# Kernel optimization log

Hardware: AMD Instinct MI355X
Metric: run time of the kernel (lower is better)

Reference implementation:

```python
import jax, jax.numpy as jnp
import numpy as np

HEADS = 4


def setup_inputs() -> dict:
    key = jax.random.key(0)
    kx, kqkv, kbq, ko, kbo = jax.random.split(key, 5)
    B, C, H, W = 4, 256, 64, 64
    x = jax.random.normal(kx, (B, C, H, W), dtype=jnp.float32)
    # torch nn.Linear stores weight as [out_features, in_features]
    w_qkv = jax.random.normal(kqkv, (3 * C, C), dtype=jnp.float32) * (1.0 / np.sqrt(C))
    b_qkv = jax.random.normal(kbq, (3 * C,), dtype=jnp.float32) * 0.02
    w_o = jax.random.normal(ko, (C, C), dtype=jnp.float32) * (1.0 / np.sqrt(C))
    b_o = jax.random.normal(kbo, (C,), dtype=jnp.float32) * 0.02
    return {"x": x, "w_qkv": w_qkv, "b_qkv": b_qkv, "w_o": w_o, "b_o": b_o}


def reference(x, w_qkv, b_qkv, w_o, b_o):
    B, C, H, W = x.shape
    S = H * W
    hd = C // HEADS
    # (B, C, H, W) -> (B, S, C)
    xt = x.reshape(B, C, S).transpose(0, 2, 1)
    qkv = xt @ w_qkv.T + b_qkv                      # (B, S, 3C)
    q, k, v = jnp.split(qkv, 3, axis=-1)
    def to_heads(t):
        return t.reshape(B, S, HEADS, hd).transpose(0, 2, 1, 3)  # (B, h, S, hd)
    q, k, v = to_heads(q), to_heads(k), to_heads(v)
    scores = jnp.einsum('bhqd,bhkd->bhqk', q, k) / jnp.sqrt(jnp.float32(hd))
    attn = jax.nn.softmax(scores, axis=-1)          # dropout inactive (eval)
    out = jnp.einsum('bhqk,bhkd->bhqd', attn, v)    # (B, h, S, hd)
    out = out.transpose(0, 2, 1, 3).reshape(B, S, C)
    y = out @ w_o.T + b_o                            # (B, S, C)
    y = y.reshape(B, H, W, C).transpose(0, 3, 1, 2)  # (B, C, H, W)
    return y
```

## Files before the change

kernel.cpp:

```cpp
#include <hip/hip_runtime.h>
#include <stdint.h>

#define DI __device__ __forceinline__

typedef __attribute__((ext_vector_type(8))) __bf16 bf16x8;
typedef __attribute__((ext_vector_type(8))) unsigned short u16x8;
typedef __attribute__((ext_vector_type(4))) float f32x4;
typedef __attribute__((ext_vector_type(4))) uint32_t u32x4;
typedef unsigned short u16;

constexpr int Bb = 4, Cc = 256, Ss = 4096, HD = 64;
constexpr int ELEMS = Bb * Cc * Ss;

DI float bf2f(u16 h) { union { unsigned u; float f; } x; x.u = ((unsigned)h) << 16; return x.f; }
DI u16 f2bf(float f) {
  union { float f; unsigned u; } x; x.f = f;
  return (u16)((x.u + 0x7FFFu + ((x.u >> 16) & 1u)) >> 16);
}
DI uint32_t pack2bf_trunc(float a, float b) {
  union { float f; uint32_t u; } xa, xb;
  xa.f = a; xb.f = b;
  return __builtin_amdgcn_perm(xb.u, xa.u, 0x07060302u);
}
DI bf16x8 ldfrag(const u16* p) { return __builtin_bit_cast(bf16x8, *(const u16x8*)p); }

DI void g2l16(const u16* g, u16* l) {
  __builtin_amdgcn_global_load_lds((const __attribute__((address_space(1))) uint32_t*)(const void*)g,
                                   (__attribute__((address_space(3))) uint32_t*)(void*)l, 16, 0, 0);
}

__global__ __launch_bounds__(256) void k_transpose(const float* __restrict__ x, u16* __restrict__ xt,
                                                   const float* __restrict__ wq, const float* __restrict__ wo,
                                                   u16* __restrict__ wqb, u16* __restrict__ wob) {
  __shared__ u16 T[64][72];
  const int st = blockIdx.x, ct = blockIdx.y, b = blockIdx.z;
  const int tid = threadIdx.x;
  {
    int flat = blockIdx.x + 64 * blockIdx.y + 256 * blockIdx.z;
    int widx = flat * 256 + tid;
    if (widx < 196608) wqb[widx] = f2bf(wq[widx]);
    else wob[widx - 196608] = f2bf(wo[widx - 196608]);
  }
#pragma unroll
  for (int e = 0; e < 2; e++) {
    int ss = tid + e * 256;
    int r = ss >> 3, seg = ss & 7;
    size_t base = ((size_t)(b * Cc + ct * 64 + r) << 12) + st * 64 + seg * 8;
    const float4* xv = (const float4*)(x + base);
    float4 v0 = xv[0], v1 = xv[1];
    u16x8 t;
    t[0] = f2bf(v0.x); t[1] = f2bf(v0.y); t[2] = f2bf(v0.z); t[3] = f2bf(v0.w);
    t[4] = f2bf(v1.x); t[5] = f2bf(v1.y); t[6] = f2bf(v1.z); t[7] = f2bf(v1.w);
    *(u16x8*)&T[r][(seg ^ ((r >> 3) & 7)) * 8] = t;
  }
  __syncthreads();
#pragma unroll
  for (int e = 0; e < 2; e++) {
    int ss = tid + e * 256;
    int sr = ss >> 3, cseg = ss & 7;
    u16x8 o;
#pragma unroll
    for (int j = 0; j < 8; j++) {
      int row = cseg * 8 + j;
      o[j] = T[row][(((sr >> 3) ^ cseg) * 8) + (sr & 7)];
    }
    *(u16x8*)(xt + ((size_t)(b * Ss + st * 64 + sr) << 8) + ct * 64 + cseg * 8) = o;
  }
}

__global__ __launch_bounds__(256) void k_qkv(const u16* __restrict__ xt, const u16* __restrict__ w,
                                             const float* __restrict__ bias,
                                             u16* __restrict__ q, u16* __restrict__ kk_, u16* __restrict__ vt) {
  __shared__ union {
    u16 ab[2][2][128][32];
    u16 tile[128][136];
  } sm;
  const int tid = threadIdx.x;
  const int wv = tid >> 6, lane = tid & 63;
  const int wm = wv >> 1, wn = wv & 1;
  const int lr = lane & 15, quad = lane >> 4;
  const int r0 = blockIdx.x * 128;
  const int j0 = blockIdx.y * 128;

  const int srow = lane >> 2;
  const int sg = ((lane & 3) ^ (srow & 3)) * 8;
  const u16* pA[2];
  const u16* pB[2];
#pragma unroll
  for (int e = 0; e < 2; e++) {
    pA[e] = xt + (size_t)(r0 + e * 64 + wv * 16 + srow) * 256 + sg;
    pB[e] = w + (size_t)(j0 + e * 64 + wv * 16 + srow) * 256 + sg;
  }
  auto stage = [&](int buf, int k0) {
#pragma unroll
    for (int e = 0; e < 2; e++) {
      g2l16(pA[e] + k0, &sm.ab[buf][0][e * 64 + wv * 16][0]);
      g2l16(pB[e] + k0, &sm.ab[buf][1][e * 64 + wv * 16][0]);
    }
  };

  f32x4 acc[4][4] = {};
  stage(0, 0);
  __syncthreads();
  for (int ks = 0; ks < 8; ks++) {
    const int cur = ks & 1;
    if (ks < 7) stage(cur ^ 1, (ks + 1) * 32);
    bf16x8 a[4], b[4];
#pragma unroll
    for (int mt = 0; mt < 4; mt++)
      a[mt] = ldfrag(&sm.ab[cur][0][wm * 64 + mt * 16 + lr][(quad ^ (lr & 3)) * 8]);
#pragma unroll
    for (int nt = 0; nt < 4; nt++)
      b[nt] = ldfrag(&sm.ab[cur][1][wn * 64 + nt * 16 + lr][(quad ^ (lr & 3)) * 8]);
#pragma unroll
    for (int mt = 0; mt < 4; mt++)
#pragma unroll
      for (int nt = 0; nt < 4; nt++)
        acc[mt][nt] = __builtin_amdgcn_mfma_f32_16x16x32_bf16(a[mt], b[nt], acc[mt][nt], 0, 0, 0);
    __syncthreads();
  }

  float bj[4];
#pragma unroll
  for (int nt = 0; nt < 4; nt++) bj[nt] = bias[j0 + wn * 64 + nt * 16 + lr];
  __syncthreads();
  if (blockIdx.y < 4) {
    const int part = blockIdx.y >> 1;
    u16* outp = part ? kk_ : q;
    const float sc = part ? 1.0f : 0.18033688f;
#pragma unroll
    for (int nt = 0; nt < 4; nt++) {
      int lc = wn * 64 + nt * 16 + lr;
#pragma unroll
      for (int mt = 0; mt < 4; mt++)
#pragma unroll
        for (int rg = 0; rg < 4; rg++)
          sm.tile[wm * 64 + mt * 16 + quad * 4 + rg][lc] = f2bf((acc[mt][nt][rg] + bj[nt]) * sc);
    }
    __syncthreads();
    const int hb2 = (blockIdx.y & 1) * 2;
#pragma unroll
    for (int it = 0; it < 8; it++) {
      int seg = tid + it * 256;
      int row = seg >> 4, cs = seg & 15;
      u16x8 o = *(const u16x8*)&sm.tile[row][cs * 8];
      int head = hb2 + (cs >> 3), d0 = (cs & 7) * 8;
      int rr = r0 + row, b_ = rr >> 12, s = rr & 4095;
      *(u16x8*)(outp + ((size_t)((b_ * 4 + head) * Ss + s) << 6) + d0) = o;
    }
  } else {
    const int hb = (blockIdx.y - 4) * 2;
#pragma unroll
    for (int nt = 0; nt < 4; nt++) {
      int lc = wn * 64 + nt * 16 + lr;
#pragma unroll
      for (int mt = 0; mt < 4; mt++)
#pragma unroll
        for (int rg = 0; rg < 4; rg++)
          sm.tile[wm * 64 + mt * 16 + quad * 4 + rg][lc] = f2bf(acc[mt][nt][rg] + bj[nt]);
    }
    __syncthreads();
    const int b2 = r0 >> 12, sbase = r0 & 4095;
#pragma unroll
    for (int it = 0; it < 8; it++) {
      int seg = tid + it * 256;
      int sq = seg & 15, hd = seg >> 4;
      int c = sq >> 3, s8 = sq & 7;
      u16x8 o;
#pragma unroll
      for (int j = 0; j < 8; j++) {
        int slot = s8 * 8 + j;
        int sw = (((slot >> 5) & 1) << 5) | (((slot >> 2) & 1) << 4) |
                 (((slot >> 3) & 3) << 2) | (slot & 3);
        o[j] = sm.tile[c * 64 + sw][hd];
      }
      int head = hb + (hd >> 6), d = hd & 63;
      *(u16x8*)(vt + ((size_t)((b2 * 4 + head) * 64 + d) << 12) + sbase + c * 64 + s8 * 8) = o;
    }
  }
}

__global__ __launch_bounds__(512, 4) void k_attn(const u16* __restrict__ Q, const u16* __restrict__ K,
                                                 const u16* __restrict__ VT, u16* __restrict__ AO,
                                                 u16* __restrict__ AOP, float* __restrict__ lpart,
                                                 int nsplit) {
  __shared__ union {
    struct { u16 Kl[2][2][64][64]; u16 Vl[2][2][64][64]; } s;
    u16 W[8][32 * 72];
  } smem;
  const int tid = threadIdx.x;
  const int wv = tid >> 6, lane = tid & 63;
  const int lr = lane & 15, quad = lane >> 4;
  const int bh = blockIdx.y;
  const int b_ = bh >> 2, head = bh & 3;
  const int qbase = blockIdx.x * 256 + wv * 32;
  const int sp = blockIdx.z;
  const int nbig = 32 / nsplit, bg0 = sp * nbig;
  const u16* Qh = Q + (size_t)bh * Ss * HD;
  const u16* Kh = K + (size_t)bh * Ss * HD;
  const u16* Vh = VT + (size_t)bh * HD * Ss;

  bf16x8 qb[2][2];
#pragma unroll
  for (int nt = 0; nt < 2; nt++)
#pragma unroll
    for (int ks = 0; ks < 2; ks++)
      qb[nt][ks] = ldfrag(Qh + (size_t)(qbase + nt * 16 + lr) * HD + ks * 32 + quad * 8);

  u16x8 ov;
#pragma unroll
  for (int j = 0; j < 8; j++) ov[j] = 0x3F80;
  const bf16x8 ones = __builtin_bit_cast(bf16x8, ov);

  f32x4 O[2][4] = {};
  f32x4 lacc[2] = {};

  const int srow = wv * 8 + (lane >> 3);
  const int sseg = ((lane & 7) ^ (lane >> 3)) * 8;
  const u16* pK = Kh + ((size_t)(bg0 * 128 + srow) << 6) + sseg;
  const u16* pV = Vh + ((size_t)srow << 12) + bg0 * 128 + sseg;
  auto stage = [&](int buf) {
#pragma unroll
    for (int s = 0; s < 2; s++) {
      g2l16(pK + (s << 12), &smem.s.Kl[buf][s][wv * 8][0]);
      g2l16(pV + s * 64, &smem.s.Vl[buf][s][wv * 8][0]);
    }
    pK += 8192; pV += 128;
  };

  stage(0);
  __syncthreads();

  for (int bc = 0; bc < nbig; bc++) {
    const int cur = bc & 1;
    if (bc + 1 < nbig) stage(cur ^ 1);

#pragma unroll
    for (int sub = 0; sub < 2; sub++) {
      u32x4 pa[2][2];
#pragma unroll
      for (int t = 0; t < 4; t++) {
        const int krow = t * 16 + lr;
        bf16x8 ka0 = ldfrag(&smem.s.Kl[cur][sub][krow][(quad ^ (lr & 7)) * 8]);
        bf16x8 ka1 = ldfrag(&smem.s.Kl[cur][sub][krow][((4 + quad) ^ (lr & 7)) * 8]);
        f32x4 St[2] = {};
        __builtin_amdgcn_s_setprio(1);
#pragma unroll
        for (int nt = 0; nt < 2; nt++)
          St[nt] = __builtin_amdgcn_mfma_f32_16x16x32_bf16(ka0, qb[nt][0], St[nt], 0, 0, 0);
#pragma unroll
        for (int nt = 0; nt < 2; nt++)
          St[nt] = __builtin_amdgcn_mfma_f32_16x16x32_bf16(ka1, qb[nt][1], St[nt], 0, 0, 0);
        __builtin_amdgcn_s_setprio(0);
        const int h = t >> 1, k2 = (t & 1) * 2;
#pragma unroll
        for (int nt = 0; nt < 2; nt++) {
          float p0 = __builtin_amdgcn_exp2f(St[nt][0]);
          float p1 = __builtin_amdgcn_exp2f(St[nt][1]);
          float p2 = __builtin_amdgcn_exp2f(St[nt][2]);
          float p3 = __builtin_amdgcn_exp2f(St[nt][3]);
          pa[h][nt][k2] = pack2bf_trunc(p0, p1);
          pa[h][nt][k2 + 1] = pack2bf_trunc(p2, p3);
        }
      }
#pragma unroll
      for (int h = 0; h < 2; h++) {
#pragma unroll
        for (int dt = 0; dt < 4; dt++) {
          bf16x8 vb = ldfrag(&smem.s.Vl[cur][sub][dt * 16 + lr][((h * 4 + quad) ^ (lr & 7)) * 8]);
          __builtin_amdgcn_s_setprio(1);
#pragma unroll
          for (int mt = 0; mt < 2; mt++)
            O[mt][dt] = __builtin_amdgcn_mfma_f32_16x16x32_bf16(
                __builtin_bit_cast(bf16x8, pa[h][mt]), vb, O[mt][dt], 0, 0, 0);
          __builtin_amdgcn_s_setprio(0);
        }
#pragma unroll
        for (int mt = 0; mt < 2; mt++)
          lacc[mt] = __builtin_amdgcn_mfma_f32_16x16x32_bf16(
              __builtin_bit_cast(bf16x8, pa[h][mt]), ones, lacc[mt], 0, 0, 0);
      }
    }
    __syncthreads();
  }

  u16* dst = (nsplit == 1) ? AO : (AOP + (size_t)sp * ELEMS);
  if (nsplit > 1 && lr == 0) {
    float* lp = lpart + (size_t)sp * (16 * Ss) + bh * Ss;
#pragma unroll
    for (int mt = 0; mt < 2; mt++)
#pragma unroll
      for (int rg = 0; rg < 4; rg++) lp[qbase + mt * 16 + quad * 4 + rg] = lacc[mt][rg];
  }
  u16* W = smem.W[wv];
#pragma unroll
  for (int mt = 0; mt < 2; mt++)
#pragma unroll
    for (int rg = 0; rg < 4; rg++) {
      float inv = 1.0f / lacc[mt][rg];
      int qq = mt * 16 + quad * 4 + rg;
#pragma unroll
      for (int dt = 0; dt < 4; dt++)
        W[qq * 72 + dt * 16 + lr] = f2bf(O[mt][dt][rg] * inv);
    }
#pragma unroll
  for (int e = 0; e < 4; e++) {
    int seg = lane + e * 64;
    int qq = seg >> 3, d0 = (seg & 7) * 8;
    u16x8 o = *(const u16x8*)&W[qq * 72 + d0];
    *(u16x8*)(dst + ((size_t)(b_ * Ss + qbase + qq) << 8) + head * 64 + d0) = o;
  }
}

__global__ __launch_bounds__(256) void k_oproj(const u16* __restrict__ wo, const u16* __restrict__ ao,
                                               const u16* __restrict__ AOP, const float* __restrict__ lpart,
                                               const float* __restrict__ bo, float* __restrict__ y, int nsplit) {
  __shared__ union {
    struct { u16 As[128][32]; u16 Bs[64][40]; } s;
    float Ys[128][68];
  } sm;
  const int tid = threadIdx.x;
  const int wv = tid >> 6, lane = tid & 63;
  const int wm = wv >> 1, wn = wv & 1;
  const int lr = lane & 15, quad = lane >> 4;
  const int n0 = blockIdx.x * 64;
  const int m0 = blockIdx.y * 128;
  const int srow = lane >> 2;
  const int sg = ((lane & 3) ^ (srow & 3)) * 8;
  const u16* pA[2];
#pragma unroll
  for (int e = 0; e < 2; e++)
    pA[e] = wo + (size_t)(m0 + e * 64 + wv * 16 + srow) * 256 + sg;
  f32x4 acc[4][2] = {};
  for (int k0 = 0; k0 < 256; k0 += 32) {
    __syncthreads();
#pragma unroll
    for (int e = 0; e < 2; e++) g2l16(pA[e] + k0, &sm.s.As[e * 64 + wv * 16][0]);
    {
      int row = tid >> 2, seg = tid & 3;
      int bs = n0 + row, cc = k0 + seg * 8;
      u16x8 t;
      if (nsplit == 1) {
        t = *(const u16x8*)(ao + ((size_t)bs << 8) + cc);
      } else {
        int b = bs >> 12, s = bs & 4095, head = cc >> 6;
        int li = (b * 4 + head) * Ss + s;
        float accv[8] = {0.f, 0.f, 0.f, 0.f, 0.f, 0.f, 0.f, 0.f};
        float lsum = 0.f;
        for (int spl = 0; spl < nsplit; spl++) {
          float l = lpart[(size_t)spl * (16 * Ss) + li];
          u16x8 a = *(const u16x8*)(AOP + (size_t)spl * ELEMS + ((size_t)bs << 8) + cc);
          lsum += l;
#pragma unroll
          for (int i = 0; i < 8; i++) accv[i] += l * bf2f(a[i]);
        }
        float inv = 1.0f / lsum;
#pragma unroll
        for (int i = 0; i < 8; i++) t[i] = f2bf(accv[i] * inv);
      }
      *(u16x8*)&sm.s.Bs[row][seg * 8] = t;
    }
    __syncthreads();
    bf16x8 a[4], b[2];
#pragma unroll
    for (int mt = 0; mt < 4; mt++)
      a[mt] = ldfrag(&sm.s.As[wm * 64 + mt * 16 + lr][(quad ^ (lr & 3)) * 8]);
#pragma unroll
    for (int nt = 0; nt < 2; nt++) b[nt] = ldfrag(&sm.s.Bs[wn * 32 + nt * 16 + lr][quad * 8]);
#pragma unroll
    for (int mt = 0; mt < 4; mt++)
#pragma unroll
      for (int nt = 0; nt < 2; nt++)
        acc[mt][nt] = __builtin_amdgcn_mfma_f32_16x16x32_bf16(a[mt], b[nt], acc[mt][nt], 0, 0, 0);
  }
  __syncthreads();
#pragma unroll
  for (int mt = 0; mt < 4; mt++)
#pragma unroll
    for (int rg = 0; rg < 4; rg++) {
      int c = wm * 64 + mt * 16 + quad * 4 + rg;
      float bc = bo[m0 + c];
#pragma unroll
      for (int nt = 0; nt < 2; nt++)
        sm.Ys[c][wn * 32 + nt * 16 + lr] = acc[mt][nt][rg] + bc;
    }
  __syncthreads();
  const int bglob = n0 >> 12, scol = n0 & 4095;
#pragma unroll
  for (int it = 0; it < 8; it++) {
    int idx = tid + it * 256;
    int row = idx >> 4, s4 = (idx & 15) * 4;
    float4 v = *(const float4*)&sm.Ys[row][s4];
    *(float4*)&y[((size_t)(bglob * Cc + m0 + row) << 12) + scol + s4] = v;
  }
}

extern "C" void kernel_launch(void* const* d_in, const int* in_sizes, int n_in,
                              void* d_out, int out_size, void* d_ws, size_t ws_size,
                              hipStream_t stream) {
  const float* x = (const float*)d_in[0];
  const float* w_qkv = (const float*)d_in[1];
  const float* b_qkv = (const float*)d_in[2];
  const float* w_o = (const float*)d_in[3];
  const float* b_o = (const float*)d_in[4];
  float* y = (float*)d_out;
  u16* ws = (u16*)d_ws;
  u16* xt = ws;
  u16* q = ws + (size_t)ELEMS;
  u16* k = ws + (size_t)2 * ELEMS;
  u16* vt = ws + (size_t)3 * ELEMS;
  u16* ao = xt;
  u16* wqb = ws + (size_t)4 * ELEMS;
  u16* wob = wqb + 196608;
  const size_t Wu16 = (size_t)4 * ELEMS + 262144;
  auto need = [&](int n) { return (Wu16 + (size_t)n * ELEMS) * 2 + (size_t)n * 16 * Ss * 4; };
  const int nsplit = (ws_size >= need(2)) ? 2 : 1;
  u16* aop = ws + Wu16;
  float* lpart = (float*)(aop + (size_t)nsplit * ELEMS);

  k_transpose<<<dim3(64, 4, 4), 256, 0, stream>>>(x, xt, w_qkv, w_o, wqb, wob);
  k_qkv<<<dim3(128, 6), 256, 0, stream>>>(xt, wqb, b_qkv, q, k, vt);
  k_attn<<<dim3(16, 16, nsplit), 512, 0, stream>>>(q, k, vt, ao, aop, lpart, nsplit);
  k_oproj<<<dim3(256, 2), 256, 0, stream>>>(wob, ao, aop, lpart, b_o, y, nsplit);
}
```

Measured before the change: 165.9 us.

## Merge oproj M-blocks into one 512-thread block with double-buffered staging; drop setprio

The output projection now computes all 256 output channels in one 512-thread block per 64-column tile instead of two 256-thread blocks. This means the split-combine of attention partials (B tile) is computed once rather than twice per column. A and B tiles are double-buffered so the next K-slice loads while MFMAs run on the current one, leaving one barrier per iteration. Separately, the s_setprio hints around the MFMAs in the attention kernel are removed. The cost is more LDS per block, fewer blocks overall, and half the threads idle while staging B.

After: 166.7 us. About the same (+0.5%).

```diff
diff --git a/kernel.cpp b/kernel.cpp
--- a/kernel.cpp
+++ b/kernel.cpp
@@ -244,14 +244,12 @@
         bf16x8 ka0 = ldfrag(&smem.s.Kl[cur][sub][krow][(quad ^ (lr & 7)) * 8]);
         bf16x8 ka1 = ldfrag(&smem.s.Kl[cur][sub][krow][((4 + quad) ^ (lr & 7)) * 8]);
         f32x4 St[2] = {};
-        __builtin_amdgcn_s_setprio(1);
 #pragma unroll
         for (int nt = 0; nt < 2; nt++)
           St[nt] = __builtin_amdgcn_mfma_f32_16x16x32_bf16(ka0, qb[nt][0], St[nt], 0, 0, 0);
 #pragma unroll
         for (int nt = 0; nt < 2; nt++)
           St[nt] = __builtin_amdgcn_mfma_f32_16x16x32_bf16(ka1, qb[nt][1], St[nt], 0, 0, 0);
-        __builtin_amdgcn_s_setprio(0);
         const int h = t >> 1, k2 = (t & 1) * 2;
 #pragma unroll
         for (int nt = 0; nt < 2; nt++) {
@@ -268,12 +266,10 @@
 #pragma unroll
         for (int dt = 0; dt < 4; dt++) {
           bf16x8 vb = ldfrag(&smem.s.Vl[cur][sub][dt * 16 + lr][((h * 4 + quad) ^ (lr & 7)) * 8]);
-          __builtin_amdgcn_s_setprio(1);
 #pragma unroll
           for (int mt = 0; mt < 2; mt++)
             O[mt][dt] = __builtin_amdgcn_mfma_f32_16x16x32_bf16(
                 __builtin_bit_cast(bf16x8, pa[h][mt]), vb, O[mt][dt], 0, 0, 0);
-          __builtin_amdgcn_s_setprio(0);
         }
 #pragma unroll
         for (int mt = 0; mt < 2; mt++)
@@ -312,31 +308,31 @@
   }
 }
 
-__global__ __launch_bounds__(256) void k_oproj(const u16* __restrict__ wo, const u16* __restrict__ ao,
+__global__ __launch_bounds__(512) void k_oproj(const u16* __restrict__ wo, const u16* __restrict__ ao,
                                                const u16* __restrict__ AOP, const float* __restrict__ lpart,
                                                const float* __restrict__ bo, float* __restrict__ y, int nsplit) {
   __shared__ union {
-    struct { u16 As[128][32]; u16 Bs[64][40]; } s;
-    float Ys[128][68];
+    struct { u16 As[2][256][32]; u16 Bs[2][64][40]; } s;
+    float Ys[256][68];
   } sm;
   const int tid = threadIdx.x;
   const int wv = tid >> 6, lane = tid & 63;
   const int wm = wv >> 1, wn = wv & 1;
   const int lr = lane & 15, quad = lane >> 4;
   const int n0 = blockIdx.x * 64;
-  const int m0 = blockIdx.y * 128;
-  const int srow = lane >> 2;
-  const int sg = ((lane & 3) ^ (srow & 3)) * 8;
+
+  const int arow = lane >> 2;
+  const int ag = ((lane & 3) ^ (arow & 3)) * 8;
   const u16* pA[2];
 #pragma unroll
   for (int e = 0; e < 2; e++)
-    pA[e] = wo + (size_t)(m0 + e * 64 + wv * 16 + srow) * 256 + sg;
-  f32x4 acc[4][2] = {};
-  for (int k0 = 0; k0 < 256; k0 += 32) {
-    __syncthreads();
-#pragma unroll
-    for (int e = 0; e < 2; e++) g2l16(pA[e] + k0, &sm.s.As[e * 64 + wv * 16][0]);
-    {
+    pA[e] = wo + (size_t)(wv * 32 + e * 16 + arow) * 256 + ag;
+  auto stageA = [&](int buf, int k0) {
+#pragma unroll
+    for (int e = 0; e < 2; e++) g2l16(pA[e] + k0, &sm.s.As[buf][wv * 32 + e * 16][0]);
+  };
+  auto stageB = [&](int buf, int k0) {
+    if (tid < 256) {
       int row = tid >> 2, seg = tid & 3;
       int bs = n0 + row, cc = k0 + seg * 8;
       u16x8 t;
@@ -358,28 +354,39 @@
 #pragma unroll
         for (int i = 0; i < 8; i++) t[i] = f2bf(accv[i] * inv);
       }
-      *(u16x8*)&sm.s.Bs[row][seg * 8] = t;
-    }
-    __syncthreads();
+      *(u16x8*)&sm.s.Bs[buf][row][seg * 8] = t;
+    }
+  };
+
+  f32x4 acc[4][2] = {};
+  stageA(0, 0);
+  stageB(0, 0);
+  __syncthreads();
+  for (int ks = 0; ks < 8; ks++) {
+    const int cur = ks & 1;
+    if (ks < 7) {
+      stageA(cur ^ 1, (ks + 1) * 32);
+      stageB(cur ^ 1, (ks + 1) * 32);
+    }
     bf16x8 a[4], b[2];
 #pragma unroll
     for (int mt = 0; mt < 4; mt++)
-      a[mt] = ldfrag(&sm.s.As[wm * 64 + mt * 16 + lr][(quad ^ (lr & 3)) * 8]);
-#pragma unroll
-    for (int nt = 0; nt < 2; nt++) b[nt] = ldfrag(&sm.s.Bs[wn * 32 + nt * 16 + lr][quad * 8]);
+      a[mt] = ldfrag(&sm.s.As[cur][wm * 64 + mt * 16 + lr][(quad ^ (lr & 3)) * 8]);
+#pragma unroll
+    for (int nt = 0; nt < 2; nt++) b[nt] = ldfrag(&sm.s.Bs[cur][wn * 32 + nt * 16 + lr][quad * 8]);
 #pragma unroll
     for (int mt = 0; mt < 4; mt++)
 #pragma unroll
       for (int nt = 0; nt < 2; nt++)
         acc[mt][nt] = __builtin_amdgcn_mfma_f32_16x16x32_bf16(a[mt], b[nt], acc[mt][nt], 0, 0, 0);
-  }
-  __syncthreads();
+    __syncthreads();
+  }
 #pragma unroll
   for (int mt = 0; mt < 4; mt++)
 #pragma unroll
     for (int rg = 0; rg < 4; rg++) {
       int c = wm * 64 + mt * 16 + quad * 4 + rg;
-      float bc = bo[m0 + c];
+      float bc = bo[c];
 #pragma unroll
       for (int nt = 0; nt < 2; nt++)
         sm.Ys[c][wn * 32 + nt * 16 + lr] = acc[mt][nt][rg] + bc;
@@ -388,10 +395,10 @@
   const int bglob = n0 >> 12, scol = n0 & 4095;
 #pragma unroll
   for (int it = 0; it < 8; it++) {
-    int idx = tid + it * 256;
+    int idx = tid + it * 512;
     int row = idx >> 4, s4 = (idx & 15) * 4;
     float4 v = *(const float4*)&sm.Ys[row][s4];
-    *(float4*)&y[((size_t)(bglob * Cc + m0 + row) << 12) + scol + s4] = v;
+    *(float4*)&y[((size_t)(bglob * Cc + row) << 12) + scol + s4] = v;
   }
 }
 
@@ -421,5 +428,5 @@
   k_transpose<<<dim3(64, 4, 4), 256, 0, stream>>>(x, xt, w_qkv, w_o, wqb, wob);
   k_qkv<<<dim3(128, 6), 256, 0, stream>>>(xt, wqb, b_qkv, q, k, vt);
   k_attn<<<dim3(16, 16, nsplit), 512, 0, stream>>>(q, k, vt, ao, aop, lpart, nsplit);
-  k_oproj<<<dim3(256, 2), 256, 0, stream>>>(wob, ao, aop, lpart, b_o, y, nsplit);
-}
+  k_oproj<<<256, 512, 0, stream>>>(wob, ao, aop, lpart, b_o, y, nsplit);
+}
```
